# Performance work log

Hardware: AMD Instinct MI355X
Metric: run time of the kernel (lower is better)

The kernel has to match this reference:

```python
import jax, jax.numpy as jnp
import numpy as np

B, L, EBDIN, NK, NC = 32768, 8, 128, 64, 10
C, D = 4, 8  # MM dims: 32//D1, D1


def _conv_relu(x, w, b):
    # x: [B,1,L,EBDIN], w: [NK,1,k,EBDIN] -> [B,NK,L-k+1,1]
    y = jax.lax.conv_general_dilated(
        x, w, window_strides=(1, 1), padding='VALID',
        dimension_numbers=('NCHW', 'OIHW', 'NCHW'))
    return jax.nn.relu(y + b[None, :, None, None])


def setup_inputs() -> dict:
    key = jax.random.key(0)
    ks = jax.random.split(key, 17)
    n = jax.random.normal
    return {
        'x': jax.random.randint(ks[0], (B, L, 2), 0, 1500, dtype=jnp.int64),
        'len_emb': n(ks[1], (1500, 16), jnp.float32),
        'ipd_emb': n(ks[2], (1500, 16), jnp.float32),
        'fc1_w': n(ks[3], (EBDIN, 32), jnp.float32) * 0.18,   # ~1/sqrt(32)
        'fc1_b': n(ks[4], (EBDIN,), jnp.float32) * 0.02,
        'S': n(ks[5], (C, D, 15), jnp.float32),
        'H': n(ks[6], (15, 16), jnp.float32),
        'T': n(ks[7], (C, 15), jnp.float32),
        'LUT': n(ks[8], (C, 16, D), jnp.float32),
        'conv3_w': n(ks[9], (NK, 1, 3, EBDIN), jnp.float32) * 0.05,
        'conv3_b': n(ks[10], (NK,), jnp.float32) * 0.02,
        'conv4_w': n(ks[11], (NK, 1, 4, EBDIN), jnp.float32) * 0.05,
        'conv4_b': n(ks[12], (NK,), jnp.float32) * 0.02,
        'conv5_w': n(ks[13], (NK, 1, 5, EBDIN), jnp.float32) * 0.05,
        'conv5_b': n(ks[14], (NK,), jnp.float32) * 0.02,
        'fc2_w': n(ks[15], (NC, 15 * NK), jnp.float32) * 0.03,
        'fc2_b': n(ks[16], (NC,), jnp.float32) * 0.02,
    }


def reference(x, len_emb, ipd_emb, fc1_w, fc1_b, S, H, T, LUT,
              conv3_w, conv3_b, conv4_w, conv4_b, conv5_w, conv5_b,
              fc2_w, fc2_b):
    b = x.shape[0]
    # embeddings + fc1 -> [b, L, EBDIN]
    e = jnp.concatenate([len_emb[x[:, :, 0]], ipd_emb[x[:, :, 1]]], axis=-1)
    h = jnp.einsum('ble,fe->blf', e, fc1_w) + fc1_b
    # MM quantization chain on flattened view [-1, C, D]
    v = h.reshape(-1, C, D)
    z = jnp.einsum('bcd,cdk->bck', v, S) - T - 1e-4
    t = jnp.tanh(z)
    ste = jax.lax.stop_gradient(jnp.sign(z) - t) + t        # sign with tanh STE
    z2 = jnp.einsum('bck,kj->bcj', ste, H)                   # [*, C, 16]
    oh = jax.nn.one_hot(jnp.argmax(z2, axis=-1), 16, dtype=z2.dtype)
    sm = jax.nn.softmax(z2, axis=-1)
    q_soft = jnp.einsum('bck,ckd->bcd', sm, LUT)
    q_hard = jnp.einsum('bck,ckd->bcd', oh, LUT)
    q = jax.lax.stop_gradient(q_hard - q_soft) + q_soft      # hard lookup, soft grad
    xq = q.reshape(b, 1, L, EBDIN)
    # three parallel convs (full-width kernels) + relu, flatten NCHW order
    f1 = _conv_relu(xq, conv3_w, conv3_b).reshape(b, -1)     # [b, NK*6]
    f2 = _conv_relu(xq, conv4_w, conv4_b).reshape(b, -1)     # [b, NK*5]
    f3 = _conv_relu(xq, conv5_w, conv5_b).reshape(b, -1)     # [b, NK*4]
    feat = jnp.concatenate([f1, f2, f3], axis=-1)            # [b, 15*NK]
    logits = feat @ fc2_w.T + fc2_b
    return jax.nn.log_softmax(logits, axis=-1), feat
```

## Files before the change

### kernel.cpp

```cpp
#include <hip/hip_runtime.h>
#include <hip/hip_bf16.h>

#define NB 32768
#define LL 8
#define EBD 128
#define NKK 64
#define FEAT 960
#define KDIM 1024

typedef __attribute__((ext_vector_type(8))) __bf16 bf16x8;
typedef __attribute__((ext_vector_type(4))) float f32x4;
typedef __attribute__((ext_vector_type(8))) unsigned short u16x8;

__global__ __launch_bounds__(256) void kq(const int* __restrict__ x,
    const float* __restrict__ len_emb, const float* __restrict__ ipd_emb,
    const float* __restrict__ fc1_w, const float* __restrict__ fc1_b,
    const float* __restrict__ S, const float* __restrict__ Hm,
    const float* __restrict__ T, const float* __restrict__ LUT,
    char* __restrict__ XQ)
{
    const int g = blockIdx.x;
    const int w = threadIdx.x >> 6, lane = threadIdx.x & 63;
    const int l = blockIdx.y * 2 + (w >> 1);
    const int half = w & 1;
    const int b0 = g * 128 + lane;
    const int p0 = b0 * 8 + l;
    const int p1 = (b0 + 64) * 8 + l;

    float e0[32], e1[32];
    {
        const float4* a0 = reinterpret_cast<const float4*>(len_emb + x[p0 * 2 + 0] * 16);
        const float4* c0 = reinterpret_cast<const float4*>(ipd_emb + x[p0 * 2 + 1] * 16);
        const float4* a1 = reinterpret_cast<const float4*>(len_emb + x[p1 * 2 + 0] * 16);
        const float4* c1 = reinterpret_cast<const float4*>(ipd_emb + x[p1 * 2 + 1] * 16);
        #pragma unroll
        for (int q = 0; q < 4; ++q) {
            float4 v = a0[q];
            e0[q * 4 + 0] = v.x; e0[q * 4 + 1] = v.y; e0[q * 4 + 2] = v.z; e0[q * 4 + 3] = v.w;
            v = c0[q];
            e0[16 + q * 4 + 0] = v.x; e0[16 + q * 4 + 1] = v.y; e0[16 + q * 4 + 2] = v.z; e0[16 + q * 4 + 3] = v.w;
            v = a1[q];
            e1[q * 4 + 0] = v.x; e1[q * 4 + 1] = v.y; e1[q * 4 + 2] = v.z; e1[q * 4 + 3] = v.w;
            v = c1[q];
            e1[16 + q * 4 + 0] = v.x; e1[16 + q * 4 + 1] = v.y; e1[16 + q * 4 + 2] = v.z; e1[16 + q * 4 + 3] = v.w;
        }
    }

    char* outbase0 = XQ + (size_t)(g * 2 + 0) * 131072 + (size_t)l * 16384 + lane * 16;
    char* outbase1 = XQ + (size_t)(g * 2 + 1) * 131072 + (size_t)l * 16384 + lane * 16;

    for (int mm = 0; mm < 8; ++mm) {
        const int m = half * 8 + mm;
        const int c = m & 3;

        float h0[8], h1[8];
        #pragma unroll
        for (int d = 0; d < 8; ++d) {
            const float* wr = fc1_w + (m * 8 + d) * 32;
            float acc0 = 0.f, acc1 = 0.f;
            #pragma unroll
            for (int j = 0; j < 32; ++j) {
                float wv = wr[j];
                acc0 += e0[j] * wv;
                acc1 += e1[j] * wv;
            }
            float bv = fc1_b[m * 8 + d];
            h0[d] = acc0 + bv;
            h1[d] = acc1 + bv;
        }

        {
            float sgn[15];
            #pragma unroll
            for (int k = 0; k < 15; ++k) {
                float z = 0.f;
                #pragma unroll
                for (int d = 0; d < 8; ++d) z += h0[d] * S[(c * 8 + d) * 15 + k];
                z = z - T[c * 15 + k];
                z = z - 1e-4f;
                sgn[k] = (z > 0.f) ? 1.f : ((z < 0.f) ? -1.f : 0.f);
            }
            float best = 0.f; int jm = 0;
            #pragma unroll
            for (int j = 0; j < 16; ++j) {
                float z2 = 0.f;
                #pragma unroll
                for (int k = 0; k < 15; ++k) z2 += sgn[k] * Hm[k * 16 + j];
                if (j == 0 || z2 > best) { best = z2; jm = j; }
            }
            const float4* lr = reinterpret_cast<const float4*>(LUT + (c * 16 + jm) * 8);
            float4 l0 = lr[0], l1 = lr[1];
            float lv[8] = {l0.x, l0.y, l0.z, l0.w, l1.x, l1.y, l1.z, l1.w};
            u16x8 pk;
            #pragma unroll
            for (int d = 0; d < 8; ++d) {
                __hip_bfloat16 t = __float2bfloat16(lv[d]);
                pk[d] = reinterpret_cast<unsigned short&>(t);
            }
            *reinterpret_cast<u16x8*>(outbase0 + m * 1024) = pk;
        }

        {
            float sgn[15];
            #pragma unroll
            for (int k = 0; k < 15; ++k) {
                float z = 0.f;
                #pragma unroll
                for (int d = 0; d < 8; ++d) z += h1[d] * S[(c * 8 + d) * 15 + k];
                z = z - T[c * 15 + k];
                z = z - 1e-4f;
                sgn[k] = (z > 0.f) ? 1.f : ((z < 0.f) ? -1.f : 0.f);
            }
            float best = 0.f; int jm = 0;
            #pragma unroll
            for (int j = 0; j < 16; ++j) {
                float z2 = 0.f;
                #pragma unroll
                for (int k = 0; k < 15; ++k) z2 += sgn[k] * Hm[k * 16 + j];
                if (j == 0 || z2 > best) { best = z2; jm = j; }
            }
            const float4* lr = reinterpret_cast<const float4*>(LUT + (c * 16 + jm) * 8);
            float4 l0 = lr[0], l1 = lr[1];
            float lv[8] = {l0.x, l0.y, l0.z, l0.w, l1.x, l1.y, l1.z, l1.w};
            u16x8 pk;
            #pragma unroll
            for (int d = 0; d < 8; ++d) {
                __hip_bfloat16 t = __float2bfloat16(lv[d]);
                pk[d] = reinterpret_cast<unsigned short&>(t);
            }
            *reinterpret_cast<u16x8*>(outbase1 + m * 1024) = pk;
        }
    }
}

__global__ __launch_bounds__(256) void km(const float* __restrict__ w3, const float* __restrict__ b3,
                                          const float* __restrict__ w4, const float* __restrict__ b4,
                                          const float* __restrict__ w5, const float* __restrict__ b5,
                                          __hip_bfloat16* __restrict__ M, float* __restrict__ bias)
{
    int id = blockIdx.x * 256 + threadIdx.x;
    if (id >= FEAT * KDIM) return;
    int j = id >> 10, k = id & 1023;
    int l = k >> 7, f = k & 127;
    float val = 0.f, bv = 0.f;
    if (j < 384) {
        int nk = j / 6, p = j % 6, i = l - p;
        if (i >= 0 && i < 3) val = w3[(nk * 3 + i) * 128 + f];
        bv = b3[nk];
    } else if (j < 704) {
        int jj = j - 384, nk = jj / 5, p = jj % 5, i = l - p;
        if (i >= 0 && i < 4) val = w4[(nk * 4 + i) * 128 + f];
        bv = b4[nk];
    } else {
        int jj = j - 704, nk = jj / 4, p = jj % 4, i = l - p;
        if (i >= 0 && i < 5) val = w5[(nk * 5 + i) * 128 + f];
        bv = b5[nk];
    }
    M[id] = __float2bfloat16(val);
    if (k == 0) bias[j] = bv;
}

#define KF_NT 16
#define KF_BUF 40960
__global__ __launch_bounds__(256) void kf(const char* __restrict__ XQg,
                                          const char* __restrict__ Mg,
                                          const float* __restrict__ bias,
                                          float* __restrict__ feat)
{
    __shared__ char smem[2 * KF_BUF];
    const int tid = threadIdx.x;
    const int lane = tid & 63, w = tid >> 6;
    const int wr = w >> 1, wc = w & 1;
    const int mrow = lane & 15, klane = lane >> 4;
    const int rowbase = blockIdx.y * 128;
    const int colbase = blockIdx.x * 192;

    auto stage = [&](int buf, int t) {
        #pragma unroll
        for (int i = 0; i < 10; ++i) {
            const int o = i * 4096 + tid * 16;
            const char* src;
            if (i < 4) {
                int bgrp = o >> 13, kc = (o >> 10) & 7, lnb_p = (o >> 4) & 63;
                int lnb = lnb_p ^ kc;
                src = XQg + ((size_t)(rowbase >> 6) + bgrp) * 131072
                          + (size_t)(t * 8 + kc) * 1024 + lnb * 16;
            } else {
                int ob = o - 16384;
                int row = ob >> 7, kwin = ob & 127;
                int kb = kwin ^ ((row & 7) << 4);
                src = Mg + (size_t)(colbase + row) * 2048 + t * 128 + kb;
            }
            char* ldst = smem + buf * KF_BUF + i * 4096 + w * 1024;
            __builtin_amdgcn_global_load_lds(
                (const __attribute__((address_space(1))) void*)src,
                (__attribute__((address_space(3))) void*)ldst,
                16, 0, 0);
        }
    };

    f32x4 acc[4][6] = {};

    stage(0, 0);
    int cur = 0;
    for (int t = 0; t < KF_NT; ++t) {
        __syncthreads();
        if (t < KF_NT - 1) stage(cur ^ 1, t + 1);

        const int abase = cur * KF_BUF;
        const int bbase = cur * KF_BUF + 16384;
        #pragma unroll
        for (int ks = 0; ks < 2; ++ks) {
            bf16x8 a[4], b[6];
            #pragma unroll
            for (int mf = 0; mf < 4; ++mf) {
                int row = wr * 64 + mf * 16 + mrow;
                int kc = ks * 4 + klane;
                a[mf] = *(const bf16x8*)(smem + abase + (row >> 6) * 8192
                                         + kc * 1024 + ((row & 63) ^ kc) * 16);
            }
            #pragma unroll
            for (int nf = 0; nf < 6; ++nf) {
                int row = wc * 96 + nf * 16 + mrow;
                int kb = ks * 64 + klane * 16;
                b[nf] = *(const bf16x8*)(smem + bbase + row * 128 + (kb ^ ((row & 7) << 4)));
            }
            #pragma unroll
            for (int mf = 0; mf < 4; ++mf)
                #pragma unroll
                for (int nf = 0; nf < 6; ++nf)
                    acc[mf][nf] = __builtin_amdgcn_mfma_f32_16x16x32_bf16(a[mf], b[nf], acc[mf][nf], 0, 0, 0);
        }
        cur ^= 1;
    }

    #pragma unroll
    for (int nf = 0; nf < 6; ++nf) {
        const int col = colbase + wc * 96 + nf * 16 + mrow;
        const float bc = bias[col];
        #pragma unroll
        for (int mf = 0; mf < 4; ++mf) {
            #pragma unroll
            for (int r = 0; r < 4; ++r) {
                int row = rowbase + wr * 64 + mf * 16 + klane * 4 + r;
                feat[(size_t)row * FEAT + col] = fmaxf(acc[mf][nf][r] + bc, 0.f);
            }
        }
    }
}

__global__ __launch_bounds__(256) void kl(const float* __restrict__ feat,
                                          const float* __restrict__ w2,
                                          const float* __restrict__ b2,
                                          float* __restrict__ out)
{
    const int b = blockIdx.x * 4 + (threadIdx.x >> 6);
    const int lane = threadIdx.x & 63;
    const float* fb = feat + (size_t)b * FEAT;

    float4 fr[4];
    #pragma unroll
    for (int p = 0; p < 4; ++p) {
        int col = p * 256 + lane * 4;
        if (p < 3 || lane < 48) fr[p] = *reinterpret_cast<const float4*>(fb + col);
        else { fr[p].x = 0.f; fr[p].y = 0.f; fr[p].z = 0.f; fr[p].w = 0.f; }
    }

    float lg[10];
    #pragma unroll
    for (int c = 0; c < 10; ++c) {
        float s = 0.f;
        #pragma unroll
        for (int p = 0; p < 4; ++p) {
            int col = p * 256 + lane * 4;
            if (p < 3 || lane < 48) {
                float4 wv = *reinterpret_cast<const float4*>(w2 + c * FEAT + col);
                s += fr[p].x * wv.x;
                s += fr[p].y * wv.y;
                s += fr[p].z * wv.z;
                s += fr[p].w * wv.w;
            }
        }
        #pragma unroll
        for (int off = 32; off >= 1; off >>= 1) s += __shfl_xor(s, off);
        lg[c] = s + b2[c];
    }
    float mx = lg[0];
    #pragma unroll
    for (int c = 1; c < 10; ++c) mx = fmaxf(mx, lg[c]);
    float se = 0.f;
    #pragma unroll
    for (int c = 0; c < 10; ++c) se += expf(lg[c] - mx);
    float ls = logf(se);
    #pragma unroll
    for (int c = 0; c < 10; ++c) if (lane == c) out[(size_t)b * 10 + c] = lg[c] - mx - ls;
}

extern "C" void kernel_launch(void* const* d_in, const int* in_sizes, int n_in,
                              void* d_out, int out_size, void* d_ws, size_t ws_size,
                              hipStream_t stream)
{
    const int*   x       = (const int*)d_in[0];
    const float* len_emb = (const float*)d_in[1];
    const float* ipd_emb = (const float*)d_in[2];
    const float* fc1_w   = (const float*)d_in[3];
    const float* fc1_b   = (const float*)d_in[4];
    const float* S       = (const float*)d_in[5];
    const float* Hm      = (const float*)d_in[6];
    const float* T       = (const float*)d_in[7];
    const float* LUT     = (const float*)d_in[8];
    const float* w3      = (const float*)d_in[9];
    const float* b3      = (const float*)d_in[10];
    const float* w4      = (const float*)d_in[11];
    const float* b4      = (const float*)d_in[12];
    const float* w5      = (const float*)d_in[13];
    const float* b5      = (const float*)d_in[14];
    const float* w2      = (const float*)d_in[15];
    const float* b2      = (const float*)d_in[16];

    char* ws = (char*)d_ws;
    char* XQ           = ws;
    __hip_bfloat16* M  = (__hip_bfloat16*)(ws + 67108864);
    float* bias        = (float*)(ws + 67108864 + 1966080);

    float* out_ls   = (float*)d_out;
    float* out_feat = (float*)d_out + NB * 10;

    hipLaunchKernelGGL(kq, dim3(NB / 128, 4), dim3(256), 0, stream,
                       x, len_emb, ipd_emb, fc1_w, fc1_b, S, Hm, T, LUT, XQ);
    hipLaunchKernelGGL(km, dim3((FEAT * KDIM + 255) / 256), dim3(256), 0, stream,
                       w3, b3, w4, b4, w5, b5, M, bias);
    hipLaunchKernelGGL(kf, dim3(5, 256), dim3(256), 0, stream,
                       XQ, (const char*)M, bias, out_feat);
    hipLaunchKernelGGL(kl, dim3(NB / 4), dim3(256), 0, stream,
                       out_feat, w2, b2, out_ls);
}
```

Baseline: 293.8 us.

## Fuse fc2 partial logits into conv GEMM epilogue with separate log-softmax reduce

The conv GEMM epilogue now multiplies its ReLU outputs by the matching fc2 weight columns and reduces them across lanes with shuffles. Each wave column writes a partial logit per row and class into a workspace buffer. A small follow-up kernel sums the ten partials, adds the bias and applies log-softmax, replacing the kernel that re-read the full 960-wide feature matrix from memory. The price is extra epilogue shuffles and register pressure in the GEMM kernel, plus a workspace-size check that falls back to the old path if the buffer is too small.

```diff
diff --git a/kernel.cpp b/kernel.cpp
--- a/kernel.cpp
+++ b/kernel.cpp
@@ -165,6 +165,8 @@
 __global__ __launch_bounds__(256) void kf(const char* __restrict__ XQg,
                                           const char* __restrict__ Mg,
                                           const float* __restrict__ bias,
+                                          const float* __restrict__ w2,
+                                          float* __restrict__ partials,
                                           float* __restrict__ feat)
 {
     __shared__ char smem[2 * KF_BUF];
@@ -243,10 +245,73 @@
             #pragma unroll
             for (int r = 0; r < 4; ++r) {
                 int row = rowbase + wr * 64 + mf * 16 + klane * 4 + r;
-                feat[(size_t)row * FEAT + col] = fmaxf(acc[mf][nf][r] + bc, 0.f);
-            }
-        }
-    }
+                float v = fmaxf(acc[mf][nf][r] + bc, 0.f);
+                acc[mf][nf][r] = v;
+                feat[(size_t)row * FEAT + col] = v;
+            }
+        }
+    }
+
+    if (partials) {
+        const int slot = blockIdx.x * 2 + wc;
+        #pragma unroll
+        for (int c = 0; c < 10; ++c) {
+            float s16[4][4];
+            #pragma unroll
+            for (int mf = 0; mf < 4; ++mf)
+                #pragma unroll
+                for (int r = 0; r < 4; ++r) s16[mf][r] = 0.f;
+            #pragma unroll
+            for (int nf = 0; nf < 6; ++nf) {
+                float wv = w2[c * FEAT + colbase + wc * 96 + nf * 16 + mrow];
+                #pragma unroll
+                for (int mf = 0; mf < 4; ++mf)
+                    #pragma unroll
+                    for (int r = 0; r < 4; ++r) s16[mf][r] += acc[mf][nf][r] * wv;
+            }
+            #pragma unroll
+            for (int off = 1; off < 16; off <<= 1) {
+                #pragma unroll
+                for (int mf = 0; mf < 4; ++mf)
+                    #pragma unroll
+                    for (int r = 0; r < 4; ++r)
+                        s16[mf][r] += __shfl_xor(s16[mf][r], off);
+            }
+            if (mrow == c) {
+                #pragma unroll
+                for (int mf = 0; mf < 4; ++mf)
+                    #pragma unroll
+                    for (int r = 0; r < 4; ++r) {
+                        int row = rowbase + wr * 64 + mf * 16 + klane * 4 + r;
+                        partials[((size_t)slot * NB + row) * 10 + c] = s16[mf][r];
+                    }
+            }
+        }
+    }
+}
+
+__global__ __launch_bounds__(256) void klsm(const float* __restrict__ partials,
+                                            const float* __restrict__ b2,
+                                            float* __restrict__ out)
+{
+    const int b = blockIdx.x * 256 + threadIdx.x;
+    float lg[10];
+    #pragma unroll
+    for (int c = 0; c < 10; ++c) lg[c] = b2[c];
+    for (int s = 0; s < 10; ++s) {
+        const float* pp = partials + ((size_t)s * NB + b) * 10;
+        #pragma unroll
+        for (int c = 0; c < 10; ++c) lg[c] += pp[c];
+    }
+    float mx = lg[0];
+    #pragma unroll
+    for (int c = 1; c < 10; ++c) mx = fmaxf(mx, lg[c]);
+    float se = 0.f;
+    #pragma unroll
+    for (int c = 0; c < 10; ++c) se += expf(lg[c] - mx);
+    float ls = logf(se);
+    #pragma unroll
+    for (int c = 0; c < 10; ++c) out[(size_t)b * 10 + c] = lg[c] - mx - ls;
 }
 
 __global__ __launch_bounds__(256) void kl(const float* __restrict__ feat,
@@ -323,6 +388,10 @@
     __hip_bfloat16* M  = (__hip_bfloat16*)(ws + 67108864);
     float* bias        = (float*)(ws + 67108864 + 1966080);
 
+    const size_t base = 69078784;
+    const size_t pbytes = (size_t)10 * NB * 10 * sizeof(float);
+    float* partials = (ws_size >= base + pbytes) ? (float*)(ws + base) : nullptr;
+
     float* out_ls   = (float*)d_out;
     float* out_feat = (float*)d_out + NB * 10;
 
@@ -331,7 +400,11 @@
     hipLaunchKernelGGL(km, dim3((FEAT * KDIM + 255) / 256), dim3(256), 0, stream,
                        w3, b3, w4, b4, w5, b5, M, bias);
     hipLaunchKernelGGL(kf, dim3(5, 256), dim3(256), 0, stream,
-                       XQ, (const char*)M, bias, out_feat);
-    hipLaunchKernelGGL(kl, dim3(NB / 4), dim3(256), 0, stream,
-                       out_feat, w2, b2, out_ls);
-}
+                       XQ, (const char*)M, bias, w2, partials, out_feat);
+    if (partials)
+        hipLaunchKernelGGL(klsm, dim3(NB / 256), dim3(256), 0, stream,
+                           partials, b2, out_ls);
+    else
+        hipLaunchKernelGGL(kl, dim3(NB / 4), dim3(256), 0, stream,
+                           out_feat, w2, b2, out_ls);
+}
```

Result: slower. 326.2 us (+11.0%).
